# Kernel optimization log

Measured on AMD Instinct MI355X. Metric: run time of the kernel, lower is better.

Reference implementation:

```python
import jax, jax.numpy as jnp
import numpy as np

B, IN, E, NCLS = 1024, 784, 256, 10
BRAIN, ADIM, NJUMPS = 4, 3, 4
N = BRAIN ** ADIM  # 64 blocks
TAU = 1.0
_GKEY = jax.random.key(42)  # fixed key -> deterministic gumbel noise


def _gumbel_softmax_hard(key, logits):
    u = jax.random.uniform(key, logits.shape, minval=1e-6, maxval=1.0 - 1e-6)
    g = -jnp.log(-jnp.log(u))
    y = jax.nn.softmax((logits + g) / TAU, axis=-1)
    hard = jax.nn.one_hot(jnp.argmax(y, axis=-1), logits.shape[-1], dtype=y.dtype)
    return jax.lax.stop_gradient(hard - y) + y  # straight-through


def _next_address(state, key, at0_W1, at0_b1, at0_W2, at0_b2):
    # always uses block 0's address_transform (as in the original forward)
    h = jax.nn.relu(state @ at0_W1 + at0_b1)
    logits = (h @ at0_W2 + at0_b2).reshape(state.shape[0], ADIM, BRAIN)
    return _gumbel_softmax_hard(key, logits)  # (B, ADIM, BRAIN) one-hot


def _all_blocks(state, st_W1, st_b1, st_W2, st_b2):
    # state: (B,E); st_W*: (N,E,E) stored (in,out). Two batched GEMMs over all N blocks.
    h = jax.nn.relu(jnp.einsum('be,neh->bnh', state, st_W1) + st_b1[None])
    h = jax.nn.relu(jnp.einsum('bnh,nhg->bng', h, st_W2) + st_b2[None])
    norm = jnp.linalg.norm(state, axis=1, keepdims=True)  # (B,1), norm of INPUT state
    return h / (norm[:, :, None] + 1e-6)  # (B,N,E)


def _flatten_onehot(oh):
    # (B, ADIM, BRAIN) -> (B, BRAIN**ADIM) via iterated outer product
    b = oh.shape[0]
    fw = oh[:, 0, :]
    for d in range(1, oh.shape[1]):
        fw = (fw[:, :, None] * oh[:, d, None, :]).reshape(b, -1)
    return fw


def _forward(x, W_emb, b_emb, st_W1, st_b1, st_W2, st_b2,
             at0_W1, at0_b1, at0_W2, at0_b2, out_W1, out_b1, out_W2, out_b2):
    bsz = x.shape[0]
    state = x.reshape(bsz, -1) @ W_emb + b_emb
    initial_state = state
    current_address = _next_address(state, jax.random.fold_in(_GKEY, 0),
                                    at0_W1, at0_b1, at0_W2, at0_b2)
    exited = jnp.zeros((bsz,), dtype=bool)
    exit_states = jnp.zeros_like(state)
    exit_addresses = jnp.zeros_like(current_address)
    for i in range(NJUMPS):  # fixed small jump count; early-break replaced by masking (same math)
        active = ~exited
        bw = _flatten_onehot(current_address)                      # (B,N)
        allout = _all_blocks(state, st_W1, st_b1, st_W2, st_b2)    # (B,N,E)
        new_state = jnp.einsum('bn,bne->be', bw, allout)
        new_address = _next_address(new_state, jax.random.fold_in(_GKEY, i + 1),
                                    at0_W1, at0_b1, at0_W2, at0_b2)
        idx = jnp.argmax(new_address, axis=2)
        is_origin = jnp.all(idx == 0, axis=1) & active
        exit_states = jnp.where(is_origin[:, None], new_state, exit_states)
        exit_addresses = jnp.where(is_origin[:, None, None], new_address, exit_addresses)
        exited = exited | is_origin
        state = jnp.where(active[:, None], new_state, state)
        current_address = jnp.where(active[:, None, None], new_address, current_address)
    final_address = jnp.where(exited[:, None, None], exit_addresses, current_address)
    bw = _flatten_onehot(final_address)
    # original code computes block_out twice and keeps the one using `state` (bug-faithful)
    allout = _all_blocks(state, st_W1, st_b1, st_W2, st_b2)
    final_output = jnp.einsum('bn,bne->be', bw, allout) + initial_state
    h = jax.nn.relu(final_output @ out_W1 + out_b1)
    return h @ out_W2 + out_b2  # (B, NCLS)


def setup_inputs() -> dict:
    key = jax.random.key(0)
    ks = jax.random.split(key, 16)
    s = 0.02
    return {
        'x': jax.random.normal(ks[0], (B, IN), jnp.float32),
        'W_emb': jax.random.normal(ks[1], (IN, E), jnp.float32) * s,
        'b_emb': jnp.zeros((E,), jnp.float32),
        'st_W1': jax.random.normal(ks[2], (N, E, E), jnp.float32) * s,
        'st_b1': jnp.zeros((N, E), jnp.float32),
        'st_W2': jax.random.normal(ks[3], (N, E, E), jnp.float32) * s,
        'st_b2': jnp.zeros((N, E), jnp.float32),
        'at0_W1': jax.random.normal(ks[4], (E, E), jnp.float32) * s,
        'at0_b1': jnp.zeros((E,), jnp.float32),
        'at0_W2': jax.random.normal(ks[5], (E, ADIM * BRAIN), jnp.float32) * s,
        'at0_b2': jnp.zeros((ADIM * BRAIN,), jnp.float32),
        'out_W1': jax.random.normal(ks[6], (E, E), jnp.float32) * s,
        'out_b1': jnp.zeros((E,), jnp.float32),
        'out_W2': jax.random.normal(ks[7], (E, NCLS), jnp.float32) * s,
        'out_b2': jnp.zeros((NCLS,), jnp.float32),
    }


def reference(x, W_emb, b_emb, st_W1, st_b1, st_W2, st_b2,
              at0_W1, at0_b1, at0_W2, at0_b2, out_W1, out_b1, out_W2, out_b2):
    return _forward(x, W_emb, b_emb, st_W1, st_b1, st_W2, st_b2,
                    at0_W1, at0_b1, at0_W2, at0_b2, out_W1, out_b1, out_W2, out_b2)
```

## Files before the change

### kernel.cpp

```cpp
#include <hip/hip_runtime.h>
#include <stdint.h>


#define BATCH 1024
#define EDIM  256
#define INDIM 784
#define GRID_BE 192

__host__ __device__ inline uint32_t rotl32(uint32_t x, uint32_t d) {
  return (x << d) | (x >> (32u - d));
}
__host__ __device__ inline void threefry2x32(uint32_t k0, uint32_t k1,
                                             uint32_t x0, uint32_t x1,
                                             uint32_t* o0, uint32_t* o1) {
  uint32_t ks2 = k0 ^ k1 ^ 0x1BD11BDAu;
  x0 += k0; x1 += k1;
#define TF_R(a) { x0 += x1; x1 = rotl32(x1, a); x1 ^= x0; }
  TF_R(13) TF_R(15) TF_R(26) TF_R(6)   x0 += k1;  x1 += ks2 + 1u;
  TF_R(17) TF_R(29) TF_R(16) TF_R(24)  x0 += ks2; x1 += k0  + 2u;
  TF_R(13) TF_R(15) TF_R(26) TF_R(6)   x0 += k0;  x1 += k1  + 3u;
  TF_R(17) TF_R(29) TF_R(16) TF_R(24)  x0 += k1;  x1 += ks2 + 4u;
  TF_R(13) TF_R(15) TF_R(26) TF_R(6)   x0 += ks2; x1 += k0  + 5u;
#undef TF_R
  *o0 = x0; *o1 = x1;
}
__device__ inline uint32_t jax_bits12288(uint32_t k0, uint32_t k1, uint32_t L) {
  uint32_t o0, o1;
  if (L < 6144u) { threefry2x32(k0, k1, L, L + 6144u, &o0, &o1); return o0; }
  else           { threefry2x32(k0, k1, L - 6144u, L, &o0, &o1); return o1; }
}
__device__ inline float jax_uniform(uint32_t bits) {
  const float minv = 1e-6f;
  const float maxv = (float)(1.0 - 1e-06);
  const float span = maxv - minv;
  uint32_t fb = (bits >> 9) | 0x3f800000u;
  float f = __uint_as_float(fb) - 1.0f;
  float u = __fadd_rn(__fmul_rn(f, span), minv);
  return fmaxf(minv, u);
}

__global__ __launch_bounds__(1024) void k_embed(
    const float* __restrict__ x, const float* __restrict__ Wemb,
    const float* __restrict__ bemb,
    float* __restrict__ stateA, float* __restrict__ initial,
    int* __restrict__ count0) {
  __shared__ float XS[8 * INDIM];
  __shared__ float P[8][128][9];
  const int t = threadIdx.x;
  if (blockIdx.x == 0 && t < 64) count0[t] = 0;
  const int rg = blockIdx.x >> 1, ch = blockIdx.x & 1;
  const int jl = t & 127, ks = t >> 7;

  {
    const float4* src = (const float4*)(x + (size_t)rg * 8 * INDIM);
    float4* dst = (float4*)XS;
    for (int p = t; p < (8 * INDIM) / 4; p += 1024) dst[p] = src[p];
  }
  __syncthreads();

  const int col = ch * 128 + jl;
  const int kb = (ks < 4) ? ks * 100 : 400 + (ks - 4) * 96;
  const int ke = kb + ((ks < 4) ? 100 : 96);
  float a[8] = {0.f,0.f,0.f,0.f,0.f,0.f,0.f,0.f};
#pragma unroll 2
  for (int k = kb; k < ke; k += 4) {
    const float w0 = Wemb[(k+0)*EDIM + col], w1 = Wemb[(k+1)*EDIM + col],
                w2 = Wemb[(k+2)*EDIM + col], w3 = Wemb[(k+3)*EDIM + col];
#pragma unroll
    for (int i = 0; i < 8; i++) {
      const float4 s4 = *(const float4*)&XS[i * INDIM + k];
      a[i] = fmaf(s4.x, w0, a[i]); a[i] = fmaf(s4.y, w1, a[i]);
      a[i] = fmaf(s4.z, w2, a[i]); a[i] = fmaf(s4.w, w3, a[i]);
    }
  }
#pragma unroll
  for (int q = 0; q < 8; q++) P[ks][jl][q] = a[q];
  __syncthreads();
  {
    const int c2 = t & 127, i = t >> 7;
    float s = 0.f;
#pragma unroll
    for (int w = 0; w < 8; w++) s += P[w][c2][i];
    s += bemb[ch * 128 + c2];
    const size_t idx = (size_t)(rg * 8 + i) * EDIM + ch * 128 + c2;
    stateA[idx] = s; initial[idx] = s;
  }
}

__global__ __launch_bounds__(1024) void k_addr(
    const float* __restrict__ state,
    const float* __restrict__ aW1, const float* __restrict__ ab1,
    const float* __restrict__ aW2, const float* __restrict__ ab2,
    int* __restrict__ exited, int* __restrict__ n_next, int* __restrict__ count,
    float* __restrict__ sout, int step, uint32_t fk0, uint32_t fk1) {
  __shared__ float XS[4 * EDIM];
  __shared__ float P[4][256][5];
  __shared__ float H[EDIM][4];
  __shared__ float P2[16][4][16];
  __shared__ float vals[4][12];
  __shared__ int   flags[4];
  const int t = threadIdx.x, b0 = blockIdx.x * 4;

  XS[t] = state[(size_t)b0 * EDIM + t];
  __syncthreads();

  const int j = t & 255, ks = t >> 8;
  const int kb = ks * 64;
  float a[4] = {0.f,0.f,0.f,0.f};
#pragma unroll 2
  for (int k = kb; k < kb + 64; k += 4) {
    const float w0 = aW1[(k+0)*EDIM + j], w1 = aW1[(k+1)*EDIM + j],
                w2 = aW1[(k+2)*EDIM + j], w3 = aW1[(k+3)*EDIM + j];
#pragma unroll
    for (int i = 0; i < 4; i++) {
      const float4 s4 = *(const float4*)&XS[i * EDIM + k];
      a[i] = fmaf(s4.x, w0, a[i]); a[i] = fmaf(s4.y, w1, a[i]);
      a[i] = fmaf(s4.z, w2, a[i]); a[i] = fmaf(s4.w, w3, a[i]);
    }
  }
#pragma unroll
  for (int q = 0; q < 4; q++) P[ks][j][q] = a[q];
  __syncthreads();
  {
    const int j2 = t & 255, i = t >> 8;
    float s = P[0][j2][i] + P[1][j2][i] + P[2][j2][i] + P[3][j2][i] + ab1[j2];
    H[j2][i] = fmaxf(s, 0.f);
  }
  __syncthreads();
  {
    const int c = t & 15, i = (t >> 4) & 3, ksl = t >> 6;
    float a2 = 0.f;
    if (c < 12) {
      const int k0 = ksl * 16;
#pragma unroll 4
      for (int k = k0; k < k0 + 16; k++)
        a2 = fmaf(H[k][i], aW2[k * 12 + c], a2);
    }
    P2[ksl][i][c] = a2;
  }
  __syncthreads();
  if (t < 48) {
    const int i = t / 12, c = t % 12;
    float s = 0.f;
#pragma unroll
    for (int w = 0; w < 16; w++) s += P2[w][i][c];
    const float logit = s + ab2[c];
    const uint32_t L = (uint32_t)((b0 + i) * 12 + c);
    const float u = jax_uniform(jax_bits12288(fk0, fk1, L));
    const float g = -logf(-logf(u));
    vals[i][c] = logit + g;
  }
  __syncthreads();
  if (t < 4) {
    const int b = b0 + t;
    int idx0 = 0, idx1 = 0, idx2 = 0;
    { float best = vals[t][0];
#pragma unroll
      for (int c = 1; c < 4; c++) { float v = vals[t][c];     if (v > best) { best = v; idx0 = c; } } }
    { float best = vals[t][4];
#pragma unroll
      for (int c = 1; c < 4; c++) { float v = vals[t][4 + c]; if (v > best) { best = v; idx1 = c; } } }
    { float best = vals[t][8];
#pragma unroll
      for (int c = 1; c < 4; c++) { float v = vals[t][8 + c]; if (v > best) { best = v; idx2 = c; } } }
    const int nn = idx0 * 16 + idx1 * 4 + idx2;
    int nxt;
    if (step == 0)      { exited[b] = 0; nxt = nn; }
    else if (step < 4)  {
      if (exited[b])      nxt = -1;
      else if (nn == 0) { exited[b] = 1; nxt = -1; }
      else                nxt = nn;
    } else                nxt = exited[b] ? 0 : nn;
    n_next[b] = nxt; flags[t] = nxt;
    if (nxt >= 0) atomicAdd(&count[nxt], 1);
  }
  __syncthreads();
  {
    const int i = t >> 8, jj = t & 255;
    if (flags[i] < 0) sout[(size_t)(b0 + i) * EDIM + jj] = XS[i * EDIM + jj];
  }
}

__global__ __launch_bounds__(1024) void k_blocks(
    const float* __restrict__ sin,
    const float* __restrict__ W1, const float* __restrict__ b1,
    const float* __restrict__ W2, const float* __restrict__ b2,
    const int* __restrict__ count, const int* __restrict__ n_next,
    const float* __restrict__ initial, float* __restrict__ sout,
    int* __restrict__ count_next, int is_final) {
  __shared__ float XS[8 * EDIM];
  __shared__ float P[4][256][9];
  __shared__ float H[EDIM][12];
  __shared__ int   meta[4];
  __shared__ int   rowsl[8];
  __shared__ float denom[8];
  __shared__ int   wcnt[16], wbase[16];
  const int t = threadIdx.x, c = blockIdx.x;
  if (c == 0 && t < 64) count_next[t] = 0;
  if (t < 8) rowsl[t] = 0;
  if (t < 64) {
    const int cnt = count[t];
    const int nch = (cnt + 7) >> 3;
    int icnt = cnt, inch = nch;
#pragma unroll
    for (int d = 1; d < 64; d <<= 1) {
      int t1 = __shfl_up(icnt, d), t2 = __shfl_up(inch, d);
      if (t >= d) { icnt += t1; inch += t2; }
    }
    const int ench = inch - nch;
    const int total = __shfl(inch, 63);
    if (t == 0) meta[3] = total;
    if (c >= ench && c < ench + nch) {
      meta[0] = t; meta[1] = c - ench;
      meta[2] = min(8, cnt - (c - ench) * 8);
    }
  }
  __syncthreads();
  if (c >= meta[3]) return;
  const int n = meta[0], local = meta[1], m = meta[2];

  {
    const bool flag = (n_next[t] == n);
    const unsigned long long bal = __ballot(flag);
    const int wid = t >> 6, lane = t & 63;
    if (lane == 0) wcnt[wid] = __popcll(bal);
    __syncthreads();
    if (t == 0) { int s = 0; for (int w = 0; w < 16; w++) { wbase[w] = s; s += wcnt[w]; } }
    __syncthreads();
    if (flag) {
      const int rank = wbase[wid] + __popcll(bal & ((1ull << lane) - 1ull));
      const int r0 = local * 8;
      if (rank >= r0 && rank < r0 + 8) rowsl[rank - r0] = t;
    }
    __syncthreads();
  }

  if (t < 512) {
    const int i = t >> 6, q = t & 63;
    const int row = rowsl[min(i, m - 1)] & 1023;
    const float4 v = *(const float4*)(sin + (size_t)row * EDIM + q * 4);
    ((float4*)XS)[t] = v;
    float sq = v.x*v.x + v.y*v.y + v.z*v.z + v.w*v.w;
#pragma unroll
    for (int d = 32; d >= 1; d >>= 1) sq += __shfl_xor(sq, d);
    if (q == 0) denom[i] = sqrtf(sq) + 1e-6f;
  }
  __syncthreads();

  const int j = t & 255, ks = t >> 8;
  const int kb = ks * 64;
  const float* W1n = W1 + (size_t)n * EDIM * EDIM;
  {
    float a[8] = {0.f,0.f,0.f,0.f,0.f,0.f,0.f,0.f};
#pragma unroll 2
    for (int k = kb; k < kb + 64; k += 4) {
      const float w0 = W1n[(k+0)*EDIM + j], w1 = W1n[(k+1)*EDIM + j],
                  w2 = W1n[(k+2)*EDIM + j], w3 = W1n[(k+3)*EDIM + j];
#pragma unroll
      for (int i = 0; i < 8; i++) {
        const float4 s4 = *(const float4*)&XS[i * EDIM + k];
        a[i] = fmaf(s4.x, w0, a[i]); a[i] = fmaf(s4.y, w1, a[i]);
        a[i] = fmaf(s4.z, w2, a[i]); a[i] = fmaf(s4.w, w3, a[i]);
      }
    }
#pragma unroll
    for (int q = 0; q < 8; q++) P[ks][j][q] = a[q];
  }
  __syncthreads();
  {
    const int j2 = t & 255, ih = t >> 8;
    const float bb = b1[(size_t)n * EDIM + j2];
#pragma unroll
    for (int qq = 0; qq < 2; qq++) {
      const int i = ih + qq * 4;
      float s = P[0][j2][i] + P[1][j2][i] + P[2][j2][i] + P[3][j2][i] + bb;
      H[j2][i] = fmaxf(s, 0.f);
    }
  }
  __syncthreads();
  const float* W2n = W2 + (size_t)n * EDIM * EDIM;
  {
    float a[8] = {0.f,0.f,0.f,0.f,0.f,0.f,0.f,0.f};
#pragma unroll 4
    for (int k = kb; k < kb + 64; k++) {
      const float w = W2n[k*EDIM + j];
      const float4 h0 = *(const float4*)&H[k][0];
      const float4 h1 = *(const float4*)&H[k][4];
      a[0] = fmaf(h0.x, w, a[0]); a[1] = fmaf(h0.y, w, a[1]);
      a[2] = fmaf(h0.z, w, a[2]); a[3] = fmaf(h0.w, w, a[3]);
      a[4] = fmaf(h1.x, w, a[4]); a[5] = fmaf(h1.y, w, a[5]);
      a[6] = fmaf(h1.z, w, a[6]); a[7] = fmaf(h1.w, w, a[7]);
    }
#pragma unroll
    for (int q = 0; q < 8; q++) P[ks][j][q] = a[q];
  }
  __syncthreads();
  {
    const int col = t & 255, ih = t >> 8;
    const float bb2 = b2[(size_t)n * EDIM + col];
#pragma unroll
    for (int qq = 0; qq < 2; qq++) {
      const int i = ih + qq * 4;
      if (i < m) {
        float s = P[0][col][i] + P[1][col][i] + P[2][col][i] + P[3][col][i] + bb2;
        float v = fmaxf(s, 0.f) / denom[i];
        const int row = rowsl[i] & 1023;
        if (is_final) v += initial[(size_t)row * EDIM + col];
        sout[(size_t)row * EDIM + col] = v;
      }
    }
  }
}

__global__ __launch_bounds__(1024) void k_head(
    const float* __restrict__ fin,
    const float* __restrict__ oW1, const float* __restrict__ ob1,
    const float* __restrict__ oW2, const float* __restrict__ ob2,
    float* __restrict__ out) {
  __shared__ float XS[4 * EDIM];
  __shared__ float P[4][256][5];
  __shared__ float H[EDIM][4];
  __shared__ float P2[16][4][16];
  const int t = threadIdx.x, b0 = blockIdx.x * 4;
  XS[t] = fin[(size_t)b0 * EDIM + t];
  __syncthreads();
  const int j = t & 255, ks = t >> 8;
  const int kb = ks * 64;
  float a[4] = {0.f,0.f,0.f,0.f};
#pragma unroll 2
  for (int k = kb; k < kb + 64; k += 4) {
    const float w0 = oW1[(k+0)*EDIM + j], w1 = oW1[(k+1)*EDIM + j],
                w2 = oW1[(k+2)*EDIM + j], w3 = oW1[(k+3)*EDIM + j];
#pragma unroll
    for (int i = 0; i < 4; i++) {
      const float4 s4 = *(const float4*)&XS[i * EDIM + k];
      a[i] = fmaf(s4.x, w0, a[i]); a[i] = fmaf(s4.y, w1, a[i]);
      a[i] = fmaf(s4.z, w2, a[i]); a[i] = fmaf(s4.w, w3, a[i]);
    }
  }
#pragma unroll
  for (int q = 0; q < 4; q++) P[ks][j][q] = a[q];
  __syncthreads();
  {
    const int j2 = t & 255, i = t >> 8;
    float s = P[0][j2][i] + P[1][j2][i] + P[2][j2][i] + P[3][j2][i] + ob1[j2];
    H[j2][i] = fmaxf(s, 0.f);
  }
  __syncthreads();
  {
    const int c = t & 15, i = (t >> 4) & 3, ksl = t >> 6;
    float a2 = 0.f;
    if (c < 10) {
      const int k0 = ksl * 16;
#pragma unroll 4
      for (int k = k0; k < k0 + 16; k++)
        a2 = fmaf(H[k][i], oW2[k * 10 + c], a2);
    }
    P2[ksl][i][c] = a2;
  }
  __syncthreads();
  if (t < 40) {
    const int i = t / 10, c = t % 10;
    float s = 0.f;
#pragma unroll
    for (int w = 0; w < 16; w++) s += P2[w][i][c];
    out[(size_t)(b0 + i) * 10 + c] = s + ob2[c];
  }
}

extern "C" void kernel_launch(void* const* d_in, const int* in_sizes, int n_in,
                              void* d_out, int out_size, void* d_ws, size_t ws_size,
                              hipStream_t stream) {
  const float* x    = (const float*)d_in[0];
  const float* Wemb = (const float*)d_in[1];
  const float* bemb = (const float*)d_in[2];
  const float* stW1 = (const float*)d_in[3];
  const float* stb1 = (const float*)d_in[4];
  const float* stW2 = (const float*)d_in[5];
  const float* stb2 = (const float*)d_in[6];
  const float* aW1  = (const float*)d_in[7];
  const float* ab1  = (const float*)d_in[8];
  const float* aW2  = (const float*)d_in[9];
  const float* ab2  = (const float*)d_in[10];
  const float* oW1  = (const float*)d_in[11];
  const float* ob1  = (const float*)d_in[12];
  const float* oW2  = (const float*)d_in[13];
  const float* ob2  = (const float*)d_in[14];
  float* out = (float*)d_out;

  char* ws = (char*)d_ws;
  auto alloc = [&](size_t bytes) { char* p = ws; ws += (bytes + 255) & ~(size_t)255; return p; };
  float* stateA  = (float*)alloc((size_t)BATCH * EDIM * 4);
  float* stateB  = (float*)alloc((size_t)BATCH * EDIM * 4);
  float* initial = (float*)alloc((size_t)BATCH * EDIM * 4);
  float* finalb  = (float*)alloc((size_t)BATCH * EDIM * 4);
  int* exited = (int*)alloc(BATCH * 4);
  int* n_next = (int*)alloc(BATCH * 4);
  int* counters[2];
  counters[0] = (int*)alloc(64 * 4);
  counters[1] = (int*)alloc(64 * 4);

  uint32_t fk0[5], fk1[5];
  for (uint32_t s = 0; s < 5; s++) threefry2x32(0u, 42u, 0u, s, &fk0[s], &fk1[s]);

  k_embed<<<256, 1024, 0, stream>>>(x, Wemb, bemb, stateA, initial, counters[0]);

  float* cur = stateA;
  float* nxt = stateB;
  for (int j = 0; j < 5; j++) {
    int* cnt  = counters[j & 1];
    int* cntN = counters[(j + 1) & 1];
    float* dst = (j < 4) ? nxt : finalb;
    k_addr<<<BATCH / 4, 1024, 0, stream>>>(cur, aW1, ab1, aW2, ab2,
        exited, n_next, cnt, dst, j, fk0[j], fk1[j]);
    k_blocks<<<GRID_BE, 1024, 0, stream>>>(cur, stW1, stb1, stW2, stb2,
        cnt, n_next, initial, dst, cntN, (j == 4) ? 1 : 0);
    if (j < 4) { float* tmp = cur; cur = nxt; nxt = tmp; }
  }
  k_head<<<BATCH / 4, 1024, 0, stream>>>(finalb, oW1, ob1, oW2, ob2, out);
}
```

Measured before the change: 265.9 us.

## Fuse embed, address, block and head kernels into one cooperative persistent kernel

Replaces the sequence of twelve separate launches (embed, five address/block step pairs, head) with a single cooperative kernel. It uses grid-wide syncs between phases and a union of per-phase shared-memory layouts. The goal is to remove per-launch overhead and inter-kernel gaps. The per-step gumbel key derivation moves from the host to the device. In exchange it pays grid.sync costs, runs every phase on 256 workgroups (the block phase now has idle extra workgroups), and depends on all workgroups being co-resident.

New measurement: 645.8 us. 2.43x slower.

```diff
diff --git a/kernel.cpp b/kernel.cpp
--- a/kernel.cpp
+++ b/kernel.cpp
@@ -1,11 +1,13 @@
 #include <hip/hip_runtime.h>
+#include <hip/hip_cooperative_groups.h>
 #include <stdint.h>
+
+namespace cg = cooperative_groups;
 
 
 #define BATCH 1024
 #define EDIM  256
 #define INDIM 784
-#define GRID_BE 192
 
 __host__ __device__ inline uint32_t rotl32(uint32_t x, uint32_t d) {
   return (x << d) | (x >> (32u - d));
@@ -39,332 +41,336 @@
   return fmaxf(minv, u);
 }
 
-__global__ __launch_bounds__(1024) void k_embed(
+struct SmemE { float XS[8 * INDIM]; float P[8][128][9]; };
+struct SmemA { float XS[4 * EDIM]; float P[4][256][5]; float H[EDIM][4];
+               float P2[16][4][16]; float vals[4][12]; int flags[4]; };
+struct SmemB { float XS[8 * EDIM]; float P[4][256][9]; float H[EDIM][12];
+               int meta[4]; int rowsl[8]; float denom[8];
+               int wcnt[16]; int wbase[16]; };
+struct SmemH { float XS[4 * EDIM]; float P[4][256][5]; float H[EDIM][4];
+               float P2[16][4][16]; };
+union Smem { SmemE e; SmemA a; SmemB b; SmemH h; };
+
+__global__ __launch_bounds__(1024, 4) void k_fused(
     const float* __restrict__ x, const float* __restrict__ Wemb,
     const float* __restrict__ bemb,
-    float* __restrict__ stateA, float* __restrict__ initial,
-    int* __restrict__ count0) {
-  __shared__ float XS[8 * INDIM];
-  __shared__ float P[8][128][9];
-  const int t = threadIdx.x;
-  if (blockIdx.x == 0 && t < 64) count0[t] = 0;
-  const int rg = blockIdx.x >> 1, ch = blockIdx.x & 1;
-  const int jl = t & 127, ks = t >> 7;
-
-  {
-    const float4* src = (const float4*)(x + (size_t)rg * 8 * INDIM);
-    float4* dst = (float4*)XS;
-    for (int p = t; p < (8 * INDIM) / 4; p += 1024) dst[p] = src[p];
-  }
-  __syncthreads();
-
-  const int col = ch * 128 + jl;
-  const int kb = (ks < 4) ? ks * 100 : 400 + (ks - 4) * 96;
-  const int ke = kb + ((ks < 4) ? 100 : 96);
-  float a[8] = {0.f,0.f,0.f,0.f,0.f,0.f,0.f,0.f};
-#pragma unroll 2
-  for (int k = kb; k < ke; k += 4) {
-    const float w0 = Wemb[(k+0)*EDIM + col], w1 = Wemb[(k+1)*EDIM + col],
-                w2 = Wemb[(k+2)*EDIM + col], w3 = Wemb[(k+3)*EDIM + col];
-#pragma unroll
-    for (int i = 0; i < 8; i++) {
-      const float4 s4 = *(const float4*)&XS[i * INDIM + k];
-      a[i] = fmaf(s4.x, w0, a[i]); a[i] = fmaf(s4.y, w1, a[i]);
-      a[i] = fmaf(s4.z, w2, a[i]); a[i] = fmaf(s4.w, w3, a[i]);
-    }
-  }
-#pragma unroll
-  for (int q = 0; q < 8; q++) P[ks][jl][q] = a[q];
-  __syncthreads();
-  {
-    const int c2 = t & 127, i = t >> 7;
-    float s = 0.f;
-#pragma unroll
-    for (int w = 0; w < 8; w++) s += P[w][c2][i];
-    s += bemb[ch * 128 + c2];
-    const size_t idx = (size_t)(rg * 8 + i) * EDIM + ch * 128 + c2;
-    stateA[idx] = s; initial[idx] = s;
-  }
-}
-
-__global__ __launch_bounds__(1024) void k_addr(
-    const float* __restrict__ state,
+    const float* __restrict__ stW1, const float* __restrict__ stb1,
+    const float* __restrict__ stW2, const float* __restrict__ stb2,
     const float* __restrict__ aW1, const float* __restrict__ ab1,
     const float* __restrict__ aW2, const float* __restrict__ ab2,
-    int* __restrict__ exited, int* __restrict__ n_next, int* __restrict__ count,
-    float* __restrict__ sout, int step, uint32_t fk0, uint32_t fk1) {
-  __shared__ float XS[4 * EDIM];
-  __shared__ float P[4][256][5];
-  __shared__ float H[EDIM][4];
-  __shared__ float P2[16][4][16];
-  __shared__ float vals[4][12];
-  __shared__ int   flags[4];
-  const int t = threadIdx.x, b0 = blockIdx.x * 4;
-
-  XS[t] = state[(size_t)b0 * EDIM + t];
-  __syncthreads();
-
-  const int j = t & 255, ks = t >> 8;
-  const int kb = ks * 64;
-  float a[4] = {0.f,0.f,0.f,0.f};
-#pragma unroll 2
-  for (int k = kb; k < kb + 64; k += 4) {
-    const float w0 = aW1[(k+0)*EDIM + j], w1 = aW1[(k+1)*EDIM + j],
-                w2 = aW1[(k+2)*EDIM + j], w3 = aW1[(k+3)*EDIM + j];
-#pragma unroll
-    for (int i = 0; i < 4; i++) {
-      const float4 s4 = *(const float4*)&XS[i * EDIM + k];
-      a[i] = fmaf(s4.x, w0, a[i]); a[i] = fmaf(s4.y, w1, a[i]);
-      a[i] = fmaf(s4.z, w2, a[i]); a[i] = fmaf(s4.w, w3, a[i]);
-    }
-  }
-#pragma unroll
-  for (int q = 0; q < 4; q++) P[ks][j][q] = a[q];
-  __syncthreads();
+    const float* __restrict__ oW1, const float* __restrict__ ob1,
+    const float* __restrict__ oW2, const float* __restrict__ ob2,
+    float* __restrict__ out,
+    float* stateA, float* stateB, float* initial, float* finalb,
+    int* exited, int* n_next, int* cnt0, int* cnt1) {
+  __shared__ Smem sm;
+  cg::grid_group grid = cg::this_grid();
+  const int t = threadIdx.x;
+  const int bid = blockIdx.x;
+
   {
-    const int j2 = t & 255, i = t >> 8;
-    float s = P[0][j2][i] + P[1][j2][i] + P[2][j2][i] + P[3][j2][i] + ab1[j2];
-    H[j2][i] = fmaxf(s, 0.f);
-  }
-  __syncthreads();
-  {
-    const int c = t & 15, i = (t >> 4) & 3, ksl = t >> 6;
-    float a2 = 0.f;
-    if (c < 12) {
-      const int k0 = ksl * 16;
-#pragma unroll 4
-      for (int k = k0; k < k0 + 16; k++)
-        a2 = fmaf(H[k][i], aW2[k * 12 + c], a2);
-    }
-    P2[ksl][i][c] = a2;
-  }
-  __syncthreads();
-  if (t < 48) {
-    const int i = t / 12, c = t % 12;
-    float s = 0.f;
-#pragma unroll
-    for (int w = 0; w < 16; w++) s += P2[w][i][c];
-    const float logit = s + ab2[c];
-    const uint32_t L = (uint32_t)((b0 + i) * 12 + c);
-    const float u = jax_uniform(jax_bits12288(fk0, fk1, L));
-    const float g = -logf(-logf(u));
-    vals[i][c] = logit + g;
-  }
-  __syncthreads();
-  if (t < 4) {
-    const int b = b0 + t;
-    int idx0 = 0, idx1 = 0, idx2 = 0;
-    { float best = vals[t][0];
-#pragma unroll
-      for (int c = 1; c < 4; c++) { float v = vals[t][c];     if (v > best) { best = v; idx0 = c; } } }
-    { float best = vals[t][4];
-#pragma unroll
-      for (int c = 1; c < 4; c++) { float v = vals[t][4 + c]; if (v > best) { best = v; idx1 = c; } } }
-    { float best = vals[t][8];
-#pragma unroll
-      for (int c = 1; c < 4; c++) { float v = vals[t][8 + c]; if (v > best) { best = v; idx2 = c; } } }
-    const int nn = idx0 * 16 + idx1 * 4 + idx2;
-    int nxt;
-    if (step == 0)      { exited[b] = 0; nxt = nn; }
-    else if (step < 4)  {
-      if (exited[b])      nxt = -1;
-      else if (nn == 0) { exited[b] = 1; nxt = -1; }
-      else                nxt = nn;
-    } else                nxt = exited[b] ? 0 : nn;
-    n_next[b] = nxt; flags[t] = nxt;
-    if (nxt >= 0) atomicAdd(&count[nxt], 1);
-  }
-  __syncthreads();
-  {
-    const int i = t >> 8, jj = t & 255;
-    if (flags[i] < 0) sout[(size_t)(b0 + i) * EDIM + jj] = XS[i * EDIM + jj];
-  }
-}
-
-__global__ __launch_bounds__(1024) void k_blocks(
-    const float* __restrict__ sin,
-    const float* __restrict__ W1, const float* __restrict__ b1,
-    const float* __restrict__ W2, const float* __restrict__ b2,
-    const int* __restrict__ count, const int* __restrict__ n_next,
-    const float* __restrict__ initial, float* __restrict__ sout,
-    int* __restrict__ count_next, int is_final) {
-  __shared__ float XS[8 * EDIM];
-  __shared__ float P[4][256][9];
-  __shared__ float H[EDIM][12];
-  __shared__ int   meta[4];
-  __shared__ int   rowsl[8];
-  __shared__ float denom[8];
-  __shared__ int   wcnt[16], wbase[16];
-  const int t = threadIdx.x, c = blockIdx.x;
-  if (c == 0 && t < 64) count_next[t] = 0;
-  if (t < 8) rowsl[t] = 0;
-  if (t < 64) {
-    const int cnt = count[t];
-    const int nch = (cnt + 7) >> 3;
-    int icnt = cnt, inch = nch;
-#pragma unroll
-    for (int d = 1; d < 64; d <<= 1) {
-      int t1 = __shfl_up(icnt, d), t2 = __shfl_up(inch, d);
-      if (t >= d) { icnt += t1; inch += t2; }
-    }
-    const int ench = inch - nch;
-    const int total = __shfl(inch, 63);
-    if (t == 0) meta[3] = total;
-    if (c >= ench && c < ench + nch) {
-      meta[0] = t; meta[1] = c - ench;
-      meta[2] = min(8, cnt - (c - ench) * 8);
-    }
-  }
-  __syncthreads();
-  if (c >= meta[3]) return;
-  const int n = meta[0], local = meta[1], m = meta[2];
-
-  {
-    const bool flag = (n_next[t] == n);
-    const unsigned long long bal = __ballot(flag);
-    const int wid = t >> 6, lane = t & 63;
-    if (lane == 0) wcnt[wid] = __popcll(bal);
-    __syncthreads();
-    if (t == 0) { int s = 0; for (int w = 0; w < 16; w++) { wbase[w] = s; s += wcnt[w]; } }
-    __syncthreads();
-    if (flag) {
-      const int rank = wbase[wid] + __popcll(bal & ((1ull << lane) - 1ull));
-      const int r0 = local * 8;
-      if (rank >= r0 && rank < r0 + 8) rowsl[rank - r0] = t;
-    }
-    __syncthreads();
-  }
-
-  if (t < 512) {
-    const int i = t >> 6, q = t & 63;
-    const int row = rowsl[min(i, m - 1)] & 1023;
-    const float4 v = *(const float4*)(sin + (size_t)row * EDIM + q * 4);
-    ((float4*)XS)[t] = v;
-    float sq = v.x*v.x + v.y*v.y + v.z*v.z + v.w*v.w;
-#pragma unroll
-    for (int d = 32; d >= 1; d >>= 1) sq += __shfl_xor(sq, d);
-    if (q == 0) denom[i] = sqrtf(sq) + 1e-6f;
-  }
-  __syncthreads();
-
-  const int j = t & 255, ks = t >> 8;
-  const int kb = ks * 64;
-  const float* W1n = W1 + (size_t)n * EDIM * EDIM;
-  {
+    if (bid == 0 && t < 64) cnt0[t] = 0;
+    const int rg = bid >> 1, ch = bid & 1;
+    const int jl = t & 127, ks = t >> 7;
+    {
+      const float4* src = (const float4*)(x + (size_t)rg * 8 * INDIM);
+      float4* dst = (float4*)sm.e.XS;
+      for (int p = t; p < (8 * INDIM) / 4; p += 1024) dst[p] = src[p];
+    }
+    __syncthreads();
+    const int col = ch * 128 + jl;
+    const int kb = (ks < 4) ? ks * 100 : 400 + (ks - 4) * 96;
+    const int ke = kb + ((ks < 4) ? 100 : 96);
     float a[8] = {0.f,0.f,0.f,0.f,0.f,0.f,0.f,0.f};
 #pragma unroll 2
-    for (int k = kb; k < kb + 64; k += 4) {
-      const float w0 = W1n[(k+0)*EDIM + j], w1 = W1n[(k+1)*EDIM + j],
-                  w2 = W1n[(k+2)*EDIM + j], w3 = W1n[(k+3)*EDIM + j];
+    for (int k = kb; k < ke; k += 4) {
+      const float w0 = Wemb[(k+0)*EDIM + col], w1 = Wemb[(k+1)*EDIM + col],
+                  w2 = Wemb[(k+2)*EDIM + col], w3 = Wemb[(k+3)*EDIM + col];
 #pragma unroll
       for (int i = 0; i < 8; i++) {
-        const float4 s4 = *(const float4*)&XS[i * EDIM + k];
+        const float4 s4 = *(const float4*)&sm.e.XS[i * INDIM + k];
         a[i] = fmaf(s4.x, w0, a[i]); a[i] = fmaf(s4.y, w1, a[i]);
         a[i] = fmaf(s4.z, w2, a[i]); a[i] = fmaf(s4.w, w3, a[i]);
       }
     }
 #pragma unroll
-    for (int q = 0; q < 8; q++) P[ks][j][q] = a[q];
+    for (int q = 0; q < 8; q++) sm.e.P[ks][jl][q] = a[q];
+    __syncthreads();
+    {
+      const int c2 = t & 127, i = t >> 7;
+      float s = 0.f;
+#pragma unroll
+      for (int w = 0; w < 8; w++) s += sm.e.P[w][c2][i];
+      s += bemb[ch * 128 + c2];
+      const size_t idx = (size_t)(rg * 8 + i) * EDIM + ch * 128 + c2;
+      stateA[idx] = s; initial[idx] = s;
+    }
   }
-  __syncthreads();
+  grid.sync();
+
+  float* cur = stateA;
+  float* nxt = stateB;
+  for (int jj = 0; jj < 5; jj++) {
+    float* dst = (jj < 4) ? nxt : finalb;
+    int* cnt  = (jj & 1) ? cnt1 : cnt0;
+    int* cntN = (jj & 1) ? cnt0 : cnt1;
+
+    {
+      const int b0 = bid * 4;
+      sm.a.XS[t] = cur[(size_t)b0 * EDIM + t];
+      __syncthreads();
+      const int j = t & 255, ks = t >> 8;
+      const int kb = ks * 64;
+      float a[4] = {0.f,0.f,0.f,0.f};
+#pragma unroll 2
+      for (int k = kb; k < kb + 64; k += 4) {
+        const float w0 = aW1[(k+0)*EDIM + j], w1 = aW1[(k+1)*EDIM + j],
+                    w2 = aW1[(k+2)*EDIM + j], w3 = aW1[(k+3)*EDIM + j];
+#pragma unroll
+        for (int i = 0; i < 4; i++) {
+          const float4 s4 = *(const float4*)&sm.a.XS[i * EDIM + k];
+          a[i] = fmaf(s4.x, w0, a[i]); a[i] = fmaf(s4.y, w1, a[i]);
+          a[i] = fmaf(s4.z, w2, a[i]); a[i] = fmaf(s4.w, w3, a[i]);
+        }
+      }
+#pragma unroll
+      for (int q = 0; q < 4; q++) sm.a.P[ks][j][q] = a[q];
+      __syncthreads();
+      {
+        const int j2 = t & 255, i = t >> 8;
+        float s = sm.a.P[0][j2][i] + sm.a.P[1][j2][i] + sm.a.P[2][j2][i]
+                + sm.a.P[3][j2][i] + ab1[j2];
+        sm.a.H[j2][i] = fmaxf(s, 0.f);
+      }
+      __syncthreads();
+      {
+        const int c = t & 15, i = (t >> 4) & 3, ksl = t >> 6;
+        float a2 = 0.f;
+        if (c < 12) {
+          const int k0 = ksl * 16;
+#pragma unroll 4
+          for (int k = k0; k < k0 + 16; k++)
+            a2 = fmaf(sm.a.H[k][i], aW2[k * 12 + c], a2);
+        }
+        sm.a.P2[ksl][i][c] = a2;
+      }
+      __syncthreads();
+      if (t < 48) {
+        const int i = t / 12, c = t % 12;
+        float s = 0.f;
+#pragma unroll
+        for (int w = 0; w < 16; w++) s += sm.a.P2[w][i][c];
+        const float logit = s + ab2[c];
+        uint32_t fk0, fk1;
+        threefry2x32(0u, 42u, 0u, (uint32_t)jj, &fk0, &fk1);
+        const uint32_t L = (uint32_t)((b0 + i) * 12 + c);
+        const float u = jax_uniform(jax_bits12288(fk0, fk1, L));
+        const float g = -logf(-logf(u));
+        sm.a.vals[i][c] = logit + g;
+      }
+      __syncthreads();
+      if (t < 4) {
+        const int b = b0 + t;
+        int idx0 = 0, idx1 = 0, idx2 = 0;
+        { float best = sm.a.vals[t][0];
+#pragma unroll
+          for (int c = 1; c < 4; c++) { float v = sm.a.vals[t][c];     if (v > best) { best = v; idx0 = c; } } }
+        { float best = sm.a.vals[t][4];
+#pragma unroll
+          for (int c = 1; c < 4; c++) { float v = sm.a.vals[t][4 + c]; if (v > best) { best = v; idx1 = c; } } }
+        { float best = sm.a.vals[t][8];
+#pragma unroll
+          for (int c = 1; c < 4; c++) { float v = sm.a.vals[t][8 + c]; if (v > best) { best = v; idx2 = c; } } }
+        const int nn = idx0 * 16 + idx1 * 4 + idx2;
+        int nxt_n;
+        if (jj == 0)      { exited[b] = 0; nxt_n = nn; }
+        else if (jj < 4)  {
+          if (exited[b])      nxt_n = -1;
+          else if (nn == 0) { exited[b] = 1; nxt_n = -1; }
+          else                nxt_n = nn;
+        } else              nxt_n = exited[b] ? 0 : nn;
+        n_next[b] = nxt_n; sm.a.flags[t] = nxt_n;
+        if (nxt_n >= 0) atomicAdd(&cnt[nxt_n], 1);
+      }
+      __syncthreads();
+      {
+        const int i = t >> 8, jc = t & 255;
+        if (sm.a.flags[i] < 0) dst[(size_t)(b0 + i) * EDIM + jc] = sm.a.XS[i * EDIM + jc];
+      }
+    }
+    grid.sync();
+
+    {
+      const int c = bid;
+      if (c == 0 && t < 64) cntN[t] = 0;
+      if (t < 8) sm.b.rowsl[t] = 0;
+      if (t < 64) {
+        const int cntv = cnt[t];
+        const int nch = (cntv + 7) >> 3;
+        int icnt = cntv, inch = nch;
+#pragma unroll
+        for (int d = 1; d < 64; d <<= 1) {
+          int t1 = __shfl_up(icnt, d), t2 = __shfl_up(inch, d);
+          if (t >= d) { icnt += t1; inch += t2; }
+        }
+        const int ench = inch - nch;
+        const int total = __shfl(inch, 63);
+        if (t == 0) sm.b.meta[3] = total;
+        if (c >= ench && c < ench + nch) {
+          sm.b.meta[0] = t; sm.b.meta[1] = c - ench;
+          sm.b.meta[2] = min(8, cntv - (c - ench) * 8);
+        }
+      }
+      __syncthreads();
+      if (c < sm.b.meta[3]) {
+        const int n = sm.b.meta[0], local = sm.b.meta[1], m = sm.b.meta[2];
+
+        {
+          const bool flag = (n_next[t] == n);
+          const unsigned long long bal = __ballot(flag);
+          const int wid = t >> 6, lane = t & 63;
+          if (lane == 0) sm.b.wcnt[wid] = __popcll(bal);
+          __syncthreads();
+          if (t == 0) { int s = 0; for (int w = 0; w < 16; w++) { sm.b.wbase[w] = s; s += sm.b.wcnt[w]; } }
+          __syncthreads();
+          if (flag) {
+            const int rank = sm.b.wbase[wid] + __popcll(bal & ((1ull << lane) - 1ull));
+            const int r0 = local * 8;
+            if (rank >= r0 && rank < r0 + 8) sm.b.rowsl[rank - r0] = t;
+          }
+          __syncthreads();
+        }
+
+        if (t < 512) {
+          const int i = t >> 6, q = t & 63;
+          const int row = sm.b.rowsl[min(i, m - 1)] & 1023;
+          const float4 v = *(const float4*)(cur + (size_t)row * EDIM + q * 4);
+          ((float4*)sm.b.XS)[t] = v;
+          float sq = v.x*v.x + v.y*v.y + v.z*v.z + v.w*v.w;
+#pragma unroll
+          for (int d = 32; d >= 1; d >>= 1) sq += __shfl_xor(sq, d);
+          if (q == 0) sm.b.denom[i] = sqrtf(sq) + 1e-6f;
+        }
+        __syncthreads();
+
+        const int j = t & 255, ks = t >> 8;
+        const int kb = ks * 64;
+        const float* W1n = stW1 + (size_t)n * EDIM * EDIM;
+        {
+          float a[8] = {0.f,0.f,0.f,0.f,0.f,0.f,0.f,0.f};
+#pragma unroll 2
+          for (int k = kb; k < kb + 64; k += 4) {
+            const float w0 = W1n[(k+0)*EDIM + j], w1 = W1n[(k+1)*EDIM + j],
+                        w2 = W1n[(k+2)*EDIM + j], w3 = W1n[(k+3)*EDIM + j];
+#pragma unroll
+            for (int i = 0; i < 8; i++) {
+              const float4 s4 = *(const float4*)&sm.b.XS[i * EDIM + k];
+              a[i] = fmaf(s4.x, w0, a[i]); a[i] = fmaf(s4.y, w1, a[i]);
+              a[i] = fmaf(s4.z, w2, a[i]); a[i] = fmaf(s4.w, w3, a[i]);
+            }
+          }
+#pragma unroll
+          for (int q = 0; q < 8; q++) sm.b.P[ks][j][q] = a[q];
+        }
+        __syncthreads();
+        {
+          const int j2 = t & 255, ih = t >> 8;
+          const float bb = stb1[(size_t)n * EDIM + j2];
+#pragma unroll
+          for (int qq = 0; qq < 2; qq++) {
+            const int i = ih + qq * 4;
+            float s = sm.b.P[0][j2][i] + sm.b.P[1][j2][i] + sm.b.P[2][j2][i]
+                    + sm.b.P[3][j2][i] + bb;
+            sm.b.H[j2][i] = fmaxf(s, 0.f);
+          }
+        }
+        __syncthreads();
+        const float* W2n = stW2 + (size_t)n * EDIM * EDIM;
+        {
+          float a[8] = {0.f,0.f,0.f,0.f,0.f,0.f,0.f,0.f};
+#pragma unroll 4
+          for (int k = kb; k < kb + 64; k++) {
+            const float w = W2n[k*EDIM + j];
+            const float4 h0 = *(const float4*)&sm.b.H[k][0];
+            const float4 h1 = *(const float4*)&sm.b.H[k][4];
+            a[0] = fmaf(h0.x, w, a[0]); a[1] = fmaf(h0.y, w, a[1]);
+            a[2] = fmaf(h0.z, w, a[2]); a[3] = fmaf(h0.w, w, a[3]);
+            a[4] = fmaf(h1.x, w, a[4]); a[5] = fmaf(h1.y, w, a[5]);
+            a[6] = fmaf(h1.z, w, a[6]); a[7] = fmaf(h1.w, w, a[7]);
+          }
+#pragma unroll
+          for (int q = 0; q < 8; q++) sm.b.P[ks][j][q] = a[q];
+        }
+        __syncthreads();
+        {
+          const int col = t & 255, ih = t >> 8;
+          const float bb2 = stb2[(size_t)n * EDIM + col];
+#pragma unroll
+          for (int qq = 0; qq < 2; qq++) {
+            const int i = ih + qq * 4;
+            if (i < m) {
+              float s = sm.b.P[0][col][i] + sm.b.P[1][col][i] + sm.b.P[2][col][i]
+                      + sm.b.P[3][col][i] + bb2;
+              float v = fmaxf(s, 0.f) / sm.b.denom[i];
+              const int row = sm.b.rowsl[i] & 1023;
+              if (jj == 4) v += initial[(size_t)row * EDIM + col];
+              dst[(size_t)row * EDIM + col] = v;
+            }
+          }
+        }
+      }
+    }
+    grid.sync();
+    if (jj < 4) { float* tmp = cur; cur = nxt; nxt = tmp; }
+  }
+
   {
-    const int j2 = t & 255, ih = t >> 8;
-    const float bb = b1[(size_t)n * EDIM + j2];
-#pragma unroll
-    for (int qq = 0; qq < 2; qq++) {
-      const int i = ih + qq * 4;
-      float s = P[0][j2][i] + P[1][j2][i] + P[2][j2][i] + P[3][j2][i] + bb;
-      H[j2][i] = fmaxf(s, 0.f);
-    }
-  }
-  __syncthreads();
-  const float* W2n = W2 + (size_t)n * EDIM * EDIM;
-  {
-    float a[8] = {0.f,0.f,0.f,0.f,0.f,0.f,0.f,0.f};
+    const int b0 = bid * 4;
+    sm.h.XS[t] = finalb[(size_t)b0 * EDIM + t];
+    __syncthreads();
+    const int j = t & 255, ks = t >> 8;
+    const int kb = ks * 64;
+    float a[4] = {0.f,0.f,0.f,0.f};
+#pragma unroll 2
+    for (int k = kb; k < kb + 64; k += 4) {
+      const float w0 = oW1[(k+0)*EDIM + j], w1 = oW1[(k+1)*EDIM + j],
+                  w2 = oW1[(k+2)*EDIM + j], w3 = oW1[(k+3)*EDIM + j];
+#pragma unroll
+      for (int i = 0; i < 4; i++) {
+        const float4 s4 = *(const float4*)&sm.h.XS[i * EDIM + k];
+        a[i] = fmaf(s4.x, w0, a[i]); a[i] = fmaf(s4.y, w1, a[i]);
+        a[i] = fmaf(s4.z, w2, a[i]); a[i] = fmaf(s4.w, w3, a[i]);
+      }
+    }
+#pragma unroll
+    for (int q = 0; q < 4; q++) sm.h.P[ks][j][q] = a[q];
+    __syncthreads();
+    {
+      const int j2 = t & 255, i = t >> 8;
+      float s = sm.h.P[0][j2][i] + sm.h.P[1][j2][i] + sm.h.P[2][j2][i]
+              + sm.h.P[3][j2][i] + ob1[j2];
+      sm.h.H[j2][i] = fmaxf(s, 0.f);
+    }
+    __syncthreads();
+    {
+      const int c = t & 15, i = (t >> 4) & 3, ksl = t >> 6;
+      float a2 = 0.f;
+      if (c < 10) {
+        const int k0 = ksl * 16;
 #pragma unroll 4
-    for (int k = kb; k < kb + 64; k++) {
-      const float w = W2n[k*EDIM + j];
-      const float4 h0 = *(const float4*)&H[k][0];
-      const float4 h1 = *(const float4*)&H[k][4];
-      a[0] = fmaf(h0.x, w, a[0]); a[1] = fmaf(h0.y, w, a[1]);
-      a[2] = fmaf(h0.z, w, a[2]); a[3] = fmaf(h0.w, w, a[3]);
-      a[4] = fmaf(h1.x, w, a[4]); a[5] = fmaf(h1.y, w, a[5]);
-      a[6] = fmaf(h1.z, w, a[6]); a[7] = fmaf(h1.w, w, a[7]);
-    }
-#pragma unroll
-    for (int q = 0; q < 8; q++) P[ks][j][q] = a[q];
-  }
-  __syncthreads();
-  {
-    const int col = t & 255, ih = t >> 8;
-    const float bb2 = b2[(size_t)n * EDIM + col];
-#pragma unroll
-    for (int qq = 0; qq < 2; qq++) {
-      const int i = ih + qq * 4;
-      if (i < m) {
-        float s = P[0][col][i] + P[1][col][i] + P[2][col][i] + P[3][col][i] + bb2;
-        float v = fmaxf(s, 0.f) / denom[i];
-        const int row = rowsl[i] & 1023;
-        if (is_final) v += initial[(size_t)row * EDIM + col];
-        sout[(size_t)row * EDIM + col] = v;
-      }
-    }
-  }
-}
-
-__global__ __launch_bounds__(1024) void k_head(
-    const float* __restrict__ fin,
-    const float* __restrict__ oW1, const float* __restrict__ ob1,
-    const float* __restrict__ oW2, const float* __restrict__ ob2,
-    float* __restrict__ out) {
-  __shared__ float XS[4 * EDIM];
-  __shared__ float P[4][256][5];
-  __shared__ float H[EDIM][4];
-  __shared__ float P2[16][4][16];
-  const int t = threadIdx.x, b0 = blockIdx.x * 4;
-  XS[t] = fin[(size_t)b0 * EDIM + t];
-  __syncthreads();
-  const int j = t & 255, ks = t >> 8;
-  const int kb = ks * 64;
-  float a[4] = {0.f,0.f,0.f,0.f};
-#pragma unroll 2
-  for (int k = kb; k < kb + 64; k += 4) {
-    const float w0 = oW1[(k+0)*EDIM + j], w1 = oW1[(k+1)*EDIM + j],
-                w2 = oW1[(k+2)*EDIM + j], w3 = oW1[(k+3)*EDIM + j];
-#pragma unroll
-    for (int i = 0; i < 4; i++) {
-      const float4 s4 = *(const float4*)&XS[i * EDIM + k];
-      a[i] = fmaf(s4.x, w0, a[i]); a[i] = fmaf(s4.y, w1, a[i]);
-      a[i] = fmaf(s4.z, w2, a[i]); a[i] = fmaf(s4.w, w3, a[i]);
-    }
-  }
-#pragma unroll
-  for (int q = 0; q < 4; q++) P[ks][j][q] = a[q];
-  __syncthreads();
-  {
-    const int j2 = t & 255, i = t >> 8;
-    float s = P[0][j2][i] + P[1][j2][i] + P[2][j2][i] + P[3][j2][i] + ob1[j2];
-    H[j2][i] = fmaxf(s, 0.f);
-  }
-  __syncthreads();
-  {
-    const int c = t & 15, i = (t >> 4) & 3, ksl = t >> 6;
-    float a2 = 0.f;
-    if (c < 10) {
-      const int k0 = ksl * 16;
-#pragma unroll 4
-      for (int k = k0; k < k0 + 16; k++)
-        a2 = fmaf(H[k][i], oW2[k * 10 + c], a2);
-    }
-    P2[ksl][i][c] = a2;
-  }
-  __syncthreads();
-  if (t < 40) {
-    const int i = t / 10, c = t % 10;
-    float s = 0.f;
-#pragma unroll
-    for (int w = 0; w < 16; w++) s += P2[w][i][c];
-    out[(size_t)(b0 + i) * 10 + c] = s + ob2[c];
+        for (int k = k0; k < k0 + 16; k++)
+          a2 = fmaf(sm.h.H[k][i], oW2[k * 10 + c], a2);
+      }
+      sm.h.P2[ksl][i][c] = a2;
+    }
+    __syncthreads();
+    if (t < 40) {
+      const int i = t / 10, c = t % 10;
+      float s = 0.f;
+#pragma unroll
+      for (int w = 0; w < 16; w++) s += sm.h.P2[w][i][c];
+      out[(size_t)(b0 + i) * 10 + c] = s + ob2[c];
+    }
   }
 }
 
@@ -396,26 +402,18 @@
   float* finalb  = (float*)alloc((size_t)BATCH * EDIM * 4);
   int* exited = (int*)alloc(BATCH * 4);
   int* n_next = (int*)alloc(BATCH * 4);
-  int* counters[2];
-  counters[0] = (int*)alloc(64 * 4);
-  counters[1] = (int*)alloc(64 * 4);
-
-  uint32_t fk0[5], fk1[5];
-  for (uint32_t s = 0; s < 5; s++) threefry2x32(0u, 42u, 0u, s, &fk0[s], &fk1[s]);
-
-  k_embed<<<256, 1024, 0, stream>>>(x, Wemb, bemb, stateA, initial, counters[0]);
-
-  float* cur = stateA;
-  float* nxt = stateB;
-  for (int j = 0; j < 5; j++) {
-    int* cnt  = counters[j & 1];
-    int* cntN = counters[(j + 1) & 1];
-    float* dst = (j < 4) ? nxt : finalb;
-    k_addr<<<BATCH / 4, 1024, 0, stream>>>(cur, aW1, ab1, aW2, ab2,
-        exited, n_next, cnt, dst, j, fk0[j], fk1[j]);
-    k_blocks<<<GRID_BE, 1024, 0, stream>>>(cur, stW1, stb1, stW2, stb2,
-        cnt, n_next, initial, dst, cntN, (j == 4) ? 1 : 0);
-    if (j < 4) { float* tmp = cur; cur = nxt; nxt = tmp; }
-  }
-  k_head<<<BATCH / 4, 1024, 0, stream>>>(finalb, oW1, ob1, oW2, ob2, out);
-}
+  int* cnt0   = (int*)alloc(64 * 4);
+  int* cnt1   = (int*)alloc(64 * 4);
+
+  void* args[] = {
+    (void*)&x, (void*)&Wemb, (void*)&bemb,
+    (void*)&stW1, (void*)&stb1, (void*)&stW2, (void*)&stb2,
+    (void*)&aW1, (void*)&ab1, (void*)&aW2, (void*)&ab2,
+    (void*)&oW1, (void*)&ob1, (void*)&oW2, (void*)&ob2,
+    (void*)&out,
+    (void*)&stateA, (void*)&stateB, (void*)&initial, (void*)&finalb,
+    (void*)&exited, (void*)&n_next, (void*)&cnt0, (void*)&cnt1
+  };
+  hipLaunchCooperativeKernel((const void*)k_fused, dim3(256), dim3(1024),
+                             args, 0, stream);
+}
```
